# Kernel optimization log

Measured on AMD Instinct MI355X. Metric: run time of the kernel, lower is better.

Reference implementation:

```python
import jax, jax.numpy as jnp
import numpy as np

# Dimensions (match init_kwargs / input_specs)
B, T, D, H, HH, E, L = 256, 512, 256, 256, 128, 32, 2


def setup_inputs() -> dict:
    key = jax.random.key(0)
    ks = jax.random.split(key, 8)
    f32 = jnp.float32
    s_ih = 1.0 / np.sqrt(D)
    s_hh = 1.0 / np.sqrt(H)
    s_hy = 1.0 / np.sqrt(D + H)
    s_hh_hy = 1.0 / np.sqrt(HH)
    s_z = 1.0 / np.sqrt(HH)
    s_d = 1.0 / np.sqrt(E)
    return {
        "input": jax.random.normal(ks[0], (B, T, D), f32),
        # main-cell weights, stacked over layers (layer1 input = hidden = D)
        "Wih": jax.random.normal(ks[1], (L, H, D), f32) * s_ih,
        "Whh": jax.random.normal(ks[2], (L, H, H), f32) * s_hh,
        "b": jnp.zeros((L, H), f32),
        # hyper (meta) RNN cell: input is concat(x_t, h_{t-1})
        "Wih_hy": jax.random.normal(ks[3], (L, HH, D + H), f32) * s_hy,
        "Whh_hy": jax.random.normal(ks[4], (L, HH, HH), f32) * s_hh_hy,
        "b_hy": jnp.zeros((L, HH), f32),
        # embedding projections: hyper_h -> z for (x-scale, h-scale, bias), then z -> d
        "Whz": jax.random.normal(ks[5], (L, 3, E, HH), f32) * s_z,
        "bz": jnp.ones((L, 3, E), f32),  # init z to 1 so d starts near a plain RNN
        "Wzd": jax.random.normal(ks[6], (L, 3, H, E), f32) * s_d,
    }


def reference(input, Wih, Whh, b, Wih_hy, Whh_hy, b_hy, Whz, bz, Wzd):
    """MetaRNN (HyperNetwork-conditioned RNN): for each layer, a small hyper RNN
    consumes [x_t, h_{t-1}] and emits embeddings z that generate per-unit scales
    d_x, d_h and a dynamic bias d_b for the main tanh RNN cell.
    Returns (all hidden states [B,T,H], last hidden state [B,H])."""
    Bb = input.shape[0]
    dt = input.dtype
    x_seq = input
    for l in range(L):
        # input-to-hidden GEMM for the whole sequence, hoisted out of the scan
        xW = jnp.einsum('btd,hd->bth', x_seq, Wih[l])  # [B,T,H]
        Whh_l, b_l = Whh[l], b[l]
        Wih_hy_l, Whh_hy_l, b_hy_l = Wih_hy[l], Whh_hy[l], b_hy[l]
        Whz_l, bz_l, Wzd_l = Whz[l], bz[l], Wzd[l]

        def step(carry, inp):
            h, hh = carry           # main hidden [B,H], hyper hidden [B,HH]
            x_t, xW_t = inp
            hyp_in = jnp.concatenate([x_t, h], axis=1)          # [B, D+H]
            hh_new = jnp.tanh(hyp_in @ Wih_hy_l.T + hh @ Whh_hy_l.T + b_hy_l)
            z = jnp.einsum('bk,gek->bge', hh_new, Whz_l) + bz_l  # [B,3,E]
            d = jnp.einsum('bge,ghe->bgh', z, Wzd_l)             # [B,3,H]
            h_new = jnp.tanh(d[:, 0] * xW_t + d[:, 1] * (h @ Whh_l.T)
                             + d[:, 2] + b_l)
            return (h_new, hh_new), h_new

        h0 = jnp.zeros((Bb, H), dt)
        hh0 = jnp.zeros((Bb, HH), dt)
        xs = (jnp.swapaxes(x_seq, 0, 1), jnp.swapaxes(xW, 0, 1))  # time-major
        _, ys = jax.lax.scan(step, (h0, hh0), xs)
        x_seq = jnp.swapaxes(ys, 0, 1)  # [B,T,H]
    return (x_seq, x_seq[:, -1, :])
```

## Files before the change

### kernel.cpp

```cpp
#include <hip/hip_runtime.h>


#define DEVI __device__ __forceinline__

typedef __bf16 bf16x8 __attribute__((ext_vector_type(8)));
typedef float f32x4 __attribute__((ext_vector_type(4)));
typedef unsigned short u16;
typedef unsigned int u32;
typedef u32 u32x4 __attribute__((ext_vector_type(4)));
typedef u16 u16x8 __attribute__((ext_vector_type(8)));

constexpr int B_ = 256, T_ = 512, D_ = 256, H_ = 256, HH_ = 128, E_ = 32;
constexpr int BT = B_ * T_;

constexpr int OXW = 0,      PXW = 16 * 8 * 512;
constexpr int OXH = 131072, PXH = 8 * 8 * 512;
constexpr int OHY = 196608, PHY = 8 * 12 * 512;
constexpr int OWHH = 294912, PWHH = 16 * 8 * 512;
constexpr int OWHZ = 425984, PWHZ = 6 * 4 * 512;
constexpr int OWZD = 450560, PWZD = 48 * 512;
constexpr int LSTRIDE = 499712;

constexpr size_t WS_XW = 0;
constexpr size_t WS_XH = (size_t)BT * H_ * 4;
constexpr size_t WS_FR = WS_XH + (size_t)BT * HH_ * 4;

DEVI u16 f2bf(float v) {
  u32 u = __float_as_uint(v);
  u += 0x7fffu + ((u >> 16) & 1u);
  return (u16)(u >> 16);
}
DEVI float bf2f(u16 s) { return __uint_as_float(((u32)s) << 16); }
DEVI void split2(float v, u16 &hi, u16 &lo) {
  hi = f2bf(v);
  lo = f2bf(v - bf2f(hi));
}
DEVI bf16x8 ldfrag(const u16 *p) {
  u32x4 v = *reinterpret_cast<const u32x4 *>(p);
  return __builtin_bit_cast(bf16x8, v);
}
DEVI void pin(bf16x8 &x) {
  u32x4 t = __builtin_bit_cast(u32x4, x);
  asm volatile("" : "+v"(t));
  x = __builtin_bit_cast(bf16x8, t);
}
DEVI f32x4 mfma3(bf16x8 ah, bf16x8 al, bf16x8 bh, bf16x8 bl, f32x4 c) {
  c = __builtin_amdgcn_mfma_f32_16x16x32_bf16(ah, bh, c, 0, 0, 0);
  c = __builtin_amdgcn_mfma_f32_16x16x32_bf16(ah, bl, c, 0, 0, 0);
  c = __builtin_amdgcn_mfma_f32_16x16x32_bf16(al, bh, c, 0, 0, 0);
  return c;
}
DEVI float tanh_fast(float x) {
  float e = __expf(2.0f * x);
  return 1.0f - 2.0f / (e + 1.0f);
}
DEVI void block_sync() {
  asm volatile("s_waitcnt lgkmcnt(0)\n\ts_barrier" ::: "memory");
}

__global__ void metarnn_prep(const float *__restrict__ Wih,
                             const float *__restrict__ Whh,
                             const float *__restrict__ Wih_hy,
                             const float *__restrict__ Whh_hy,
                             const float *__restrict__ Whz,
                             const float *__restrict__ Wzd,
                             u16 *__restrict__ fr) {
  int gid = blockIdx.x * 256 + threadIdx.x;
  int lane = gid & 63;
  int e = gid >> 6;
  if (e >= 2 * 488) return;
  int l = e / 488, r = e - l * 488;
  u16 *base = fr + (size_t)l * LSTRIDE;
  int rowL = lane & 15, kg = (lane >> 4) << 3;

  const float *src = nullptr;
  int ld = 0, nt = 0, kt = 0, KT = 1, special = 0;
  u16 *dh = nullptr, *dl = nullptr;
  if (r < 128) {
    nt = r >> 3; kt = r & 7; KT = 8;
    src = Wih + (size_t)l * H_ * D_; ld = D_;
    dh = base + OXW; dl = dh + PXW;
  } else if (r < 192) {
    r -= 128; nt = r >> 3; kt = r & 7; KT = 8;
    src = Wih_hy + (size_t)l * HH_ * (D_ + H_); ld = D_ + H_;
    dh = base + OXH; dl = dh + PXH;
  } else if (r < 288) {
    r -= 192; nt = r / 12; kt = r - nt * 12; KT = 12; special = 1;
    dh = base + OHY; dl = dh + PHY;
  } else if (r < 416) {
    r -= 288; nt = r >> 3; kt = r & 7; KT = 8;
    src = Whh + (size_t)l * H_ * H_; ld = H_;
    dh = base + OWHH; dl = dh + PWHH;
  } else if (r < 440) {
    r -= 416; nt = r >> 2; kt = r & 3; KT = 4;
    src = Whz + (size_t)l * 3 * E_ * HH_; ld = HH_;
    dh = base + OWHZ; dl = dh + PWHZ;
  } else {
    r -= 440; int g = r >> 4; nt = r & 15; kt = 0; KT = 1;
    src = Wzd + (size_t)(l * 3 + g) * H_ * E_; ld = E_;
    dh = base + OWZD + g * 16 * 512; dl = base + OWZD + PWZD + g * 16 * 512;
  }
  int row = nt * 16 + rowL;
  long dof = ((long)(nt * KT + kt) * 64 + lane) * 8;
  for (int j = 0; j < 8; ++j) {
    int k = kt * 32 + kg + j;
    float v;
    if (special) {
      v = (k < 256) ? Wih_hy[((size_t)l * HH_ + row) * (D_ + H_) + 256 + k]
                    : Whh_hy[((size_t)l * HH_ + row) * HH_ + (k - 256)];
    } else {
      v = src[(size_t)row * ld + k];
    }
    u16 hi, lo;
    split2(v, hi, lo);
    dh[dof + j] = hi;
    dl[dof + j] = lo;
  }
}

__global__ __launch_bounds__(256, 1) void metarnn_gemm(
    const float *__restrict__ x, const u16 *__restrict__ fr,
    float *__restrict__ xW, float *__restrict__ xH) {
  int w = threadIdx.x >> 6, lane = threadIdx.x & 63;
  int m0 = blockIdx.x * 32;
  int rowL = lane & 15, kg = (lane >> 4) << 3;
  f32x4 acc[2][6] = {};
  const u16 *fxw_h = fr + OXW, *fxw_l = fxw_h + PXW;
  const u16 *fxh_h = fr + OXH, *fxh_l = fxh_h + PXH;

  for (int kt = 0; kt < 8; ++kt) {
    bf16x8 ah[2], al[2];
    for (int s = 0; s < 2; ++s) {
      const float *xp = x + (size_t)(m0 + s * 16 + rowL) * 256 + kt * 32 + kg;
      u16x8 vh, vl;
#pragma unroll
      for (int j = 0; j < 8; ++j) {
        u16 hi, lo;
        split2(xp[j], hi, lo);
        vh[j] = hi; vl[j] = lo;
      }
      ah[s] = __builtin_bit_cast(bf16x8, vh);
      al[s] = __builtin_bit_cast(bf16x8, vl);
    }
#pragma unroll
    for (int q = 0; q < 6; ++q) {
      int nt = w * 6 + q;
      long o = (nt < 16) ? ((long)(nt * 8 + kt) * 64 + lane) * 8
                         : ((long)((nt - 16) * 8 + kt) * 64 + lane) * 8;
      const u16 *bh = (nt < 16) ? fxw_h + o : fxh_h + o;
      const u16 *bl = (nt < 16) ? fxw_l + o : fxh_l + o;
      bf16x8 B0 = ldfrag(bh), B1 = ldfrag(bl);
      acc[0][q] = mfma3(ah[0], al[0], B0, B1, acc[0][q]);
      acc[1][q] = mfma3(ah[1], al[1], B0, B1, acc[1][q]);
    }
  }
  for (int s = 0; s < 2; ++s)
    for (int q = 0; q < 6; ++q) {
      int nt = w * 6 + q;
#pragma unroll
      for (int r = 0; r < 4; ++r) {
        int row = m0 + s * 16 + (lane >> 4) * 4 + r;
        if (nt < 16)
          xW[(size_t)row * H_ + nt * 16 + rowL] = acc[s][q][r];
        else
          xH[(size_t)row * HH_ + (nt - 16) * 16 + rowL] = acc[s][q][r];
      }
    }
}

__global__ __launch_bounds__(512, 2) void metarnn_scan(
    const float *__restrict__ xW, const float *__restrict__ xH,
    const u16 *__restrict__ fr, const float *__restrict__ bmain,
    const float *__restrict__ bhy, const float *__restrict__ bz,
    float *__restrict__ y, float *__restrict__ hlast, int layer, int isLast) {
  __shared__ __align__(16) u16 hc_h[8 * 512];
  __shared__ __align__(16) u16 hc_l[8 * 512];
  __shared__ __align__(16) u16 hhb_h[2][4 * 512];
  __shared__ __align__(16) u16 hhb_l[2][4 * 512];
  __shared__ __align__(16) u16 zf_h[3 * 512];
  __shared__ __align__(16) u16 zf_l[3 * 512];
  __shared__ __align__(16) u16 hy_lds[8 * 12 * 512];

  int tid = threadIdx.x, w = tid >> 6, lane = tid & 63;
  int bs = blockIdx.x * 16;
  int rowL = lane & 15, colG = lane >> 4;

  const u16 *FHY = fr + OHY, *FHYl = FHY + PHY;
  const u16 *FWH = fr + OWHH, *FWHl = FWH + PWHH;
  const u16 *FWZ = fr + OWHZ, *FWZl = FWZ + PWHZ;
  const u16 *FZD = fr + OWZD, *FZDl = FZD + PWZD;

  for (int i = tid; i < 8 * 512; i += 512) { hc_h[i] = 0; hc_l[i] = 0; }
  for (int i = tid; i < 4 * 512; i += 512) {
    hhb_h[0][i] = 0; hhb_l[0][i] = 0; hhb_h[1][i] = 0; hhb_l[1][i] = 0;
  }
  for (int i = tid; i < 3 * 512; i += 512) { zf_h[i] = 0; zf_l[i] = 0; }
  for (int i = tid; i < 8 * 12 * 512 / 8; i += 512) {
    *reinterpret_cast<u32x4 *>(&hy_lds[(size_t)i * 8]) =
        *reinterpret_cast<const u32x4 *>(FHY + (size_t)i * 8);
  }

  bf16x8 RWH[2][8], RWL[2][8];
#pragma unroll
  for (int p = 0; p < 2; ++p)
#pragma unroll
    for (int kt = 0; kt < 8; ++kt) {
      long o = ((long)((2 * w + p) * 8 + kt) * 64 + lane) * 8;
      RWH[p][kt] = ldfrag(FWH + o);  pin(RWH[p][kt]);
      RWL[p][kt] = ldfrag(FWHl + o); pin(RWL[p][kt]);
    }
  bf16x8 zresH[4], zresL[4];
  {
    int wz = (w < 6) ? w : 0;
#pragma unroll
    for (int kk = 0; kk < 4; ++kk) {
      long o = ((long)(wz * 4 + kk) * 64 + lane) * 8;
      zresH[kk] = ldfrag(FWZ + o);  pin(zresH[kk]);
      zresL[kk] = ldfrag(FWZl + o); pin(zresL[kk]);
    }
  }

  int c2 = 16 * w + rowL;
  float bhv = bhy[layer * HH_ + c2];
  float bzv = (w < 6) ? bz[layer * 3 * E_ + c2] : 0.0f;
  float bbv[2];
  bbv[0] = bmain[layer * H_ + 32 * w + rowL];
  bbv[1] = bmain[layer * H_ + 32 * w + 16 + rowL];

  bf16x8 bYL[4];
#define LOAD_Y(PTR, S, KT)                                                    \
  bYL[S] = ldfrag((PTR) + ((long)(w * 12 + (KT)) * 64 + lane) * 8);
#pragma unroll
  for (int s = 0; s < 4; ++s) { LOAD_Y(FHYl, s, s) }

  float xhv[4], xwv[2][4];
#pragma unroll
  for (int r = 0; r < 4; ++r) {
    size_t row = (size_t)(bs + 4 * colG + r) * T_;
    xhv[r] = xH[row * HH_ + c2];
    xwv[0][r] = xW[row * H_ + 32 * w + rowL];
    xwv[1][r] = xW[row * H_ + 32 * w + 16 + rowL];
  }

  __syncthreads();

  for (int t = 0; t < T_; ++t) {
    const int pr = t & 1;
    const u16 *fhyl = FHYl, *fzd = FZD, *fzdl = FZDl;
    asm volatile("" : "+s"(fhyl), "+s"(fzd), "+s"(fzdl));

    f32x4 aAe = {}, aAo = {}, aW0 = {}, aW1 = {};
    __builtin_amdgcn_s_setprio(1);
#pragma unroll
    for (int j = 0; j < 12; ++j) {
      const int s4 = j & 3;
      bf16x8 ah, al;
      if (j < 8) {
        ah = ldfrag(&hc_h[j * 512 + lane * 8]);
        al = ldfrag(&hc_l[j * 512 + lane * 8]);
      } else {
        ah = ldfrag(&hhb_h[pr ^ 1][(j - 8) * 512 + lane * 8]);
        al = ldfrag(&hhb_l[pr ^ 1][(j - 8) * 512 + lane * 8]);
      }
      bf16x8 yh = ldfrag(&hy_lds[(w * 12 + j) * 512 + lane * 8]);
      if (j & 1) aAo = mfma3(ah, al, yh, bYL[s4], aAo);
      else       aAe = mfma3(ah, al, yh, bYL[s4], aAe);
      if (j < 8) {
        aW0 = mfma3(ah, al, RWH[0][j], RWL[0][j], aW0);
        aW1 = mfma3(ah, al, RWH[1][j], RWL[1][j], aW1);
        LOAD_Y(fhyl, s4, j + 4)
      } else {
        LOAD_Y(fhyl, s4, j - 8)
      }
    }
    __builtin_amdgcn_s_setprio(0);
    f32x4 aA;
#pragma unroll
    for (int r = 0; r < 4; ++r) aA[r] = aAe[r] + aAo[r];

    bf16x8 D0h[2], D0l[2];
#pragma unroll
    for (int p = 0; p < 2; ++p) {
      long o = ((long)(2 * w + p) * 64 + lane) * 8;
      D0h[p] = ldfrag(fzd + o);
      D0l[p] = ldfrag(fzdl + o);
    }

    {
      int kfr = w >> 1;
      int hb2 = 2 * (w & 1) + (rowL >> 3);
      int j7 = rowL & 7;
#pragma unroll
      for (int r = 0; r < 4; ++r) {
        float v = tanh_fast(aA[r] + xhv[r] + bhv);
        u16 hi, lo;
        split2(v, hi, lo);
        int di = kfr * 512 + ((4 * colG + r) + 16 * hb2) * 8 + j7;
        hhb_h[pr][di] = hi;
        hhb_l[pr][di] = lo;
      }
    }
#pragma unroll
    for (int r = 0; r < 4; ++r) {
      xhv[r] = xH[((size_t)(bs + 4 * colG + r) * T_ + t + 1) * HH_ + c2];
    }
    block_sync();

    bf16x8 D1h[2], D1l[2], D2h[2], D2l[2];
#pragma unroll
    for (int p = 0; p < 2; ++p) {
      long o1 = ((long)(16 + 2 * w + p) * 64 + lane) * 8;
      long o2 = ((long)(32 + 2 * w + p) * 64 + lane) * 8;
      D1h[p] = ldfrag(fzd + o1);
      D1l[p] = ldfrag(fzdl + o1);
      D2h[p] = ldfrag(fzd + o2);
      D2l[p] = ldfrag(fzdl + o2);
    }

    if (w < 6) {
      f32x4 aZ = {};
#pragma unroll
      for (int kk = 0; kk < 4; ++kk) {
        bf16x8 ah = ldfrag(&hhb_h[pr][kk * 512 + lane * 8]);
        bf16x8 al = ldfrag(&hhb_l[pr][kk * 512 + lane * 8]);
        aZ = mfma3(ah, al, zresH[kk], zresL[kk], aZ);
      }
      int g = c2 >> 5;
      int hb3 = 2 * (w & 1) + (rowL >> 3);
      int j7 = rowL & 7;
#pragma unroll
      for (int r = 0; r < 4; ++r) {
        float v = aZ[r] + bzv;
        u16 hi, lo;
        split2(v, hi, lo);
        int di = g * 512 + ((4 * colG + r) + 16 * hb3) * 8 + j7;
        zf_h[di] = hi;
        zf_l[di] = lo;
      }
    }
    block_sync();

    float arg[2][4];
#pragma unroll
    for (int p = 0; p < 2; ++p)
#pragma unroll
      for (int r = 0; r < 4; ++r) arg[p][r] = bbv[p];
    {
      bf16x8 zh = ldfrag(&zf_h[0 * 512 + lane * 8]);
      bf16x8 zl = ldfrag(&zf_l[0 * 512 + lane * 8]);
#pragma unroll
      for (int p = 0; p < 2; ++p) {
        f32x4 zero = {};
        f32x4 dg = mfma3(zh, zl, D0h[p], D0l[p], zero);
#pragma unroll
        for (int r = 0; r < 4; ++r) arg[p][r] += dg[r] * xwv[p][r];
      }
    }
#pragma unroll
    for (int r = 0; r < 4; ++r) {
      size_t row = (size_t)(bs + 4 * colG + r) * T_ + t + 1;
      xwv[0][r] = xW[row * H_ + 32 * w + rowL];
      xwv[1][r] = xW[row * H_ + 32 * w + 16 + rowL];
    }
    {
      bf16x8 zh = ldfrag(&zf_h[1 * 512 + lane * 8]);
      bf16x8 zl = ldfrag(&zf_l[1 * 512 + lane * 8]);
#pragma unroll
      for (int p = 0; p < 2; ++p) {
        f32x4 zero = {};
        f32x4 dg = mfma3(zh, zl, D1h[p], D1l[p], zero);
#pragma unroll
        for (int r = 0; r < 4; ++r)
          arg[p][r] += dg[r] * ((p == 0) ? aW0[r] : aW1[r]);
      }
    }
    {
      bf16x8 zh = ldfrag(&zf_h[2 * 512 + lane * 8]);
      bf16x8 zl = ldfrag(&zf_l[2 * 512 + lane * 8]);
#pragma unroll
      for (int p = 0; p < 2; ++p) {
        f32x4 zero = {};
        f32x4 dg = mfma3(zh, zl, D2h[p], D2l[p], zero);
#pragma unroll
        for (int r = 0; r < 4; ++r) arg[p][r] += dg[r];
      }
    }

#pragma unroll
    for (int p = 0; p < 2; ++p) {
      int c = 32 * w + 16 * p + rowL;
      int hb6 = 2 * p + (rowL >> 3);
      int j7 = rowL & 7;
#pragma unroll
      for (int r = 0; r < 4; ++r) {
        int m = 4 * colG + r;
        float h = tanh_fast(arg[p][r]);
        size_t gi = (size_t)(bs + m) * T_ + t;
        y[gi * H_ + c] = h;
        if (isLast && t == T_ - 1) hlast[(size_t)(bs + m) * H_ + c] = h;
        u16 hi, lo;
        split2(h, hi, lo);
        int di = (c >> 5) * 512 + (m + 16 * hb6) * 8 + j7;
        hc_h[di] = hi;
        hc_l[di] = lo;
      }
    }
    block_sync();
  }
#undef LOAD_Y
}

extern "C" void kernel_launch(void *const *d_in, const int *in_sizes, int n_in,
                              void *d_out, int out_size, void *d_ws,
                              size_t ws_size, hipStream_t stream) {
  (void)in_sizes; (void)n_in; (void)out_size; (void)ws_size;
  const float *input  = (const float *)d_in[0];
  const float *Wih    = (const float *)d_in[1];
  const float *Whh    = (const float *)d_in[2];
  const float *b      = (const float *)d_in[3];
  const float *Wih_hy = (const float *)d_in[4];
  const float *Whh_hy = (const float *)d_in[5];
  const float *b_hy   = (const float *)d_in[6];
  const float *Whz    = (const float *)d_in[7];
  const float *bz     = (const float *)d_in[8];
  const float *Wzd    = (const float *)d_in[9];

  float *out = (float *)d_out;
  float *xW = (float *)((char *)d_ws + WS_XW);
  float *xH = (float *)((char *)d_ws + WS_XH);
  u16 *fr = (u16 *)((char *)d_ws + WS_FR);
  float *hlast = out + (size_t)BT * H_;

  metarnn_prep<<<dim3(244), dim3(256), 0, stream>>>(Wih, Whh, Wih_hy, Whh_hy,
                                                    Whz, Wzd, fr);
  for (int l = 0; l < 2; ++l) {
    const float *xsrc = (l == 0) ? input : out;
    const u16 *frl = fr + (size_t)l * LSTRIDE;
    metarnn_gemm<<<dim3(BT / 32), dim3(256), 0, stream>>>(xsrc, frl, xW, xH);
    metarnn_scan<<<dim3(16), dim3(512), 0, stream>>>(
        xW, xH, frl, b, b_hy, bz, out, hlast, l, (l == 1) ? 1 : 0);
  }
}
```

Baseline: 9.273 ms.

## Keep hyper weights in registers, move Whz hi to LDS, split weights inline in gemm

The scan kernel now holds all 12 low-part hyper-RNN weight fragments in registers instead of streaming them from global memory each step. The Whz high part moves into LDS and its low part is reloaded per step rather than pinned, and the Wzd fragment loads are spread across phases to reduce register pressure. The input GEMM now reads fp32 weights directly and splits them into bf16 hi/lo pairs inline, which removes the prep work and workspace for those matrices. This shifts register and LDS budgets inside the latency-bound recurrent loop and adds conversion work to the GEMM.

```diff
diff --git a/kernel.cpp b/kernel.cpp
--- a/kernel.cpp
+++ b/kernel.cpp
@@ -13,13 +13,11 @@
 constexpr int B_ = 256, T_ = 512, D_ = 256, H_ = 256, HH_ = 128, E_ = 32;
 constexpr int BT = B_ * T_;
 
-constexpr int OXW = 0,      PXW = 16 * 8 * 512;
-constexpr int OXH = 131072, PXH = 8 * 8 * 512;
-constexpr int OHY = 196608, PHY = 8 * 12 * 512;
-constexpr int OWHH = 294912, PWHH = 16 * 8 * 512;
-constexpr int OWHZ = 425984, PWHZ = 6 * 4 * 512;
-constexpr int OWZD = 450560, PWZD = 48 * 512;
-constexpr int LSTRIDE = 499712;
+constexpr int OHY = 0,       PHY = 8 * 12 * 512;
+constexpr int OWHH = 98304,  PWHH = 16 * 8 * 512;
+constexpr int OWHZ = 229376, PWHZ = 6 * 4 * 512;
+constexpr int OWZD = 253952, PWZD = 48 * 512;
+constexpr int LSTRIDE = 303104;
 
 constexpr size_t WS_XW = 0;
 constexpr size_t WS_XH = (size_t)BT * H_ * 4;
@@ -58,8 +56,7 @@
   asm volatile("s_waitcnt lgkmcnt(0)\n\ts_barrier" ::: "memory");
 }
 
-__global__ void metarnn_prep(const float *__restrict__ Wih,
-                             const float *__restrict__ Whh,
+__global__ void metarnn_prep(const float *__restrict__ Whh,
                              const float *__restrict__ Wih_hy,
                              const float *__restrict__ Whh_hy,
                              const float *__restrict__ Whz,
@@ -68,65 +65,76 @@
   int gid = blockIdx.x * 256 + threadIdx.x;
   int lane = gid & 63;
   int e = gid >> 6;
-  if (e >= 2 * 488) return;
-  int l = e / 488, r = e - l * 488;
+  if (e >= 2 * 296) return;
+  int l = e / 296, r = e - l * 296;
   u16 *base = fr + (size_t)l * LSTRIDE;
   int rowL = lane & 15, kg = (lane >> 4) << 3;
 
-  const float *src = nullptr;
-  int ld = 0, nt = 0, kt = 0, KT = 1, special = 0;
-  u16 *dh = nullptr, *dl = nullptr;
-  if (r < 128) {
-    nt = r >> 3; kt = r & 7; KT = 8;
-    src = Wih + (size_t)l * H_ * D_; ld = D_;
-    dh = base + OXW; dl = dh + PXW;
-  } else if (r < 192) {
-    r -= 128; nt = r >> 3; kt = r & 7; KT = 8;
-    src = Wih_hy + (size_t)l * HH_ * (D_ + H_); ld = D_ + H_;
-    dh = base + OXH; dl = dh + PXH;
-  } else if (r < 288) {
-    r -= 192; nt = r / 12; kt = r - nt * 12; KT = 12; special = 1;
-    dh = base + OHY; dl = dh + PHY;
-  } else if (r < 416) {
-    r -= 288; nt = r >> 3; kt = r & 7; KT = 8;
-    src = Whh + (size_t)l * H_ * H_; ld = H_;
-    dh = base + OWHH; dl = dh + PWHH;
-  } else if (r < 440) {
-    r -= 416; nt = r >> 2; kt = r & 3; KT = 4;
-    src = Whz + (size_t)l * 3 * E_ * HH_; ld = HH_;
-    dh = base + OWHZ; dl = dh + PWHZ;
+  if (r < 96) {
+    int nt = r / 12, kt = r - nt * 12;
+    u16 *dh = base + OHY, *dl = dh + PHY;
+    int row = nt * 16 + rowL;
+    long dof = ((long)(nt * 12 + kt) * 64 + lane) * 8;
+    for (int j = 0; j < 8; ++j) {
+      int k = kt * 32 + kg + j;
+      float v = (k < 256)
+                    ? Wih_hy[((size_t)l * HH_ + row) * (D_ + H_) + 256 + k]
+                    : Whh_hy[((size_t)l * HH_ + row) * HH_ + (k - 256)];
+      u16 hi, lo;
+      split2(v, hi, lo);
+      dh[dof + j] = hi;
+      dl[dof + j] = lo;
+    }
+  } else if (r < 224) {
+    int m = r - 96;
+    int nt = m >> 3, kt = m & 7;
+    u16 *dh = base + OWHH, *dl = dh + PWHH;
+    int row = nt * 16 + rowL;
+    long dof = ((long)(nt * 8 + kt) * 64 + lane) * 8;
+    const float *src = Whh + (size_t)l * H_ * H_;
+    for (int j = 0; j < 8; ++j) {
+      u16 hi, lo;
+      split2(src[(size_t)row * H_ + kt * 32 + kg + j], hi, lo);
+      dh[dof + j] = hi;
+      dl[dof + j] = lo;
+    }
+  } else if (r < 248) {
+    int m = r - 224;
+    int nt = m >> 2, kt = m & 3;
+    u16 *dh = base + OWHZ, *dl = dh + PWHZ;
+    int row = nt * 16 + rowL;
+    long dof = ((long)(nt * 4 + kt) * 64 + lane) * 8;
+    const float *src = Whz + (size_t)l * 3 * E_ * HH_;
+    for (int j = 0; j < 8; ++j) {
+      u16 hi, lo;
+      split2(src[(size_t)row * HH_ + kt * 32 + kg + j], hi, lo);
+      dh[dof + j] = hi;
+      dl[dof + j] = lo;
+    }
   } else {
-    r -= 440; int g = r >> 4; nt = r & 15; kt = 0; KT = 1;
-    src = Wzd + (size_t)(l * 3 + g) * H_ * E_; ld = E_;
-    dh = base + OWZD + g * 16 * 512; dl = base + OWZD + PWZD + g * 16 * 512;
-  }
-  int row = nt * 16 + rowL;
-  long dof = ((long)(nt * KT + kt) * 64 + lane) * 8;
-  for (int j = 0; j < 8; ++j) {
-    int k = kt * 32 + kg + j;
-    float v;
-    if (special) {
-      v = (k < 256) ? Wih_hy[((size_t)l * HH_ + row) * (D_ + H_) + 256 + k]
-                    : Whh_hy[((size_t)l * HH_ + row) * HH_ + (k - 256)];
-    } else {
-      v = src[(size_t)row * ld + k];
-    }
-    u16 hi, lo;
-    split2(v, hi, lo);
-    dh[dof + j] = hi;
-    dl[dof + j] = lo;
+    int m = r - 248;
+    int g = m >> 4, nt = m & 15;
+    u16 *dh = base + OWZD + g * 16 * 512, *dl = dh + PWZD;
+    int row = nt * 16 + rowL;
+    long dof = ((long)nt * 64 + lane) * 8;
+    const float *src = Wzd + (size_t)(l * 3 + g) * H_ * E_;
+    for (int j = 0; j < 8; ++j) {
+      u16 hi, lo;
+      split2(src[(size_t)row * E_ + kg + j], hi, lo);
+      dh[dof + j] = hi;
+      dl[dof + j] = lo;
+    }
   }
 }
 
 __global__ __launch_bounds__(256, 1) void metarnn_gemm(
-    const float *__restrict__ x, const u16 *__restrict__ fr,
-    float *__restrict__ xW, float *__restrict__ xH) {
+    const float *__restrict__ x, const float *__restrict__ Wih_l,
+    const float *__restrict__ Why_l, float *__restrict__ xW,
+    float *__restrict__ xH) {
   int w = threadIdx.x >> 6, lane = threadIdx.x & 63;
   int m0 = blockIdx.x * 32;
   int rowL = lane & 15, kg = (lane >> 4) << 3;
   f32x4 acc[2][6] = {};
-  const u16 *fxw_h = fr + OXW, *fxw_l = fxw_h + PXW;
-  const u16 *fxh_h = fr + OXH, *fxh_l = fxh_h + PXH;
 
   for (int kt = 0; kt < 8; ++kt) {
     bf16x8 ah[2], al[2];
@@ -145,11 +153,18 @@
 #pragma unroll
     for (int q = 0; q < 6; ++q) {
       int nt = w * 6 + q;
-      long o = (nt < 16) ? ((long)(nt * 8 + kt) * 64 + lane) * 8
-                         : ((long)((nt - 16) * 8 + kt) * 64 + lane) * 8;
-      const u16 *bh = (nt < 16) ? fxw_h + o : fxh_h + o;
-      const u16 *bl = (nt < 16) ? fxw_l + o : fxh_l + o;
-      bf16x8 B0 = ldfrag(bh), B1 = ldfrag(bl);
+      const float *wp = (nt < 16)
+          ? Wih_l + (size_t)(nt * 16 + rowL) * 256 + kt * 32 + kg
+          : Why_l + (size_t)((nt - 16) * 16 + rowL) * 512 + kt * 32 + kg;
+      u16x8 vbh, vbl;
+#pragma unroll
+      for (int j = 0; j < 8; ++j) {
+        u16 hi, lo;
+        split2(wp[j], hi, lo);
+        vbh[j] = hi; vbl[j] = lo;
+      }
+      bf16x8 B0 = __builtin_bit_cast(bf16x8, vbh);
+      bf16x8 B1 = __builtin_bit_cast(bf16x8, vbl);
       acc[0][q] = mfma3(ah[0], al[0], B0, B1, acc[0][q]);
       acc[1][q] = mfma3(ah[1], al[1], B0, B1, acc[1][q]);
     }
@@ -180,6 +195,7 @@
   __shared__ __align__(16) u16 zf_h[3 * 512];
   __shared__ __align__(16) u16 zf_l[3 * 512];
   __shared__ __align__(16) u16 hy_lds[8 * 12 * 512];
+  __shared__ __align__(16) u16 whz_lds[6 * 4 * 512];
 
   int tid = threadIdx.x, w = tid >> 6, lane = tid & 63;
   int bs = blockIdx.x * 16;
@@ -199,6 +215,10 @@
     *reinterpret_cast<u32x4 *>(&hy_lds[(size_t)i * 8]) =
         *reinterpret_cast<const u32x4 *>(FHY + (size_t)i * 8);
   }
+  for (int i = tid; i < 6 * 4 * 512 / 8; i += 512) {
+    *reinterpret_cast<u32x4 *>(&whz_lds[(size_t)i * 8]) =
+        *reinterpret_cast<const u32x4 *>(FWZ + (size_t)i * 8);
+  }
 
   bf16x8 RWH[2][8], RWL[2][8];
 #pragma unroll
@@ -209,30 +229,21 @@
       RWH[p][kt] = ldfrag(FWH + o);  pin(RWH[p][kt]);
       RWL[p][kt] = ldfrag(FWHl + o); pin(RWL[p][kt]);
     }
-  bf16x8 zresH[4], zresL[4];
-  {
-    int wz = (w < 6) ? w : 0;
-#pragma unroll
-    for (int kk = 0; kk < 4; ++kk) {
-      long o = ((long)(wz * 4 + kk) * 64 + lane) * 8;
-      zresH[kk] = ldfrag(FWZ + o);  pin(zresH[kk]);
-      zresL[kk] = ldfrag(FWZl + o); pin(zresL[kk]);
-    }
+  bf16x8 RYL[12];
+#pragma unroll
+  for (int j = 0; j < 12; ++j) {
+    RYL[j] = ldfrag(FHYl + ((long)(w * 12 + j) * 64 + lane) * 8);
+    pin(RYL[j]);
   }
 
   int c2 = 16 * w + rowL;
+  int wz = (w < 6) ? w : 0;
   float bhv = bhy[layer * HH_ + c2];
   float bzv = (w < 6) ? bz[layer * 3 * E_ + c2] : 0.0f;
   float bbv[2];
   bbv[0] = bmain[layer * H_ + 32 * w + rowL];
   bbv[1] = bmain[layer * H_ + 32 * w + 16 + rowL];
 
-  bf16x8 bYL[4];
-#define LOAD_Y(PTR, S, KT)                                                    \
-  bYL[S] = ldfrag((PTR) + ((long)(w * 12 + (KT)) * 64 + lane) * 8);
-#pragma unroll
-  for (int s = 0; s < 4; ++s) { LOAD_Y(FHYl, s, s) }
-
   float xhv[4], xwv[2][4];
 #pragma unroll
   for (int r = 0; r < 4; ++r) {
@@ -246,14 +257,11 @@
 
   for (int t = 0; t < T_; ++t) {
     const int pr = t & 1;
-    const u16 *fhyl = FHYl, *fzd = FZD, *fzdl = FZDl;
-    asm volatile("" : "+s"(fhyl), "+s"(fzd), "+s"(fzdl));
-
+    const int tn = (t + 1 < T_) ? t + 1 : t;
     f32x4 aAe = {}, aAo = {}, aW0 = {}, aW1 = {};
     __builtin_amdgcn_s_setprio(1);
 #pragma unroll
     for (int j = 0; j < 12; ++j) {
-      const int s4 = j & 3;
       bf16x8 ah, al;
       if (j < 8) {
         ah = ldfrag(&hc_h[j * 512 + lane * 8]);
@@ -263,14 +271,11 @@
         al = ldfrag(&hhb_l[pr ^ 1][(j - 8) * 512 + lane * 8]);
       }
       bf16x8 yh = ldfrag(&hy_lds[(w * 12 + j) * 512 + lane * 8]);
-      if (j & 1) aAo = mfma3(ah, al, yh, bYL[s4], aAo);
-      else       aAe = mfma3(ah, al, yh, bYL[s4], aAe);
+      if (j & 1) aAo = mfma3(ah, al, yh, RYL[j], aAo);
+      else       aAe = mfma3(ah, al, yh, RYL[j], aAe);
       if (j < 8) {
         aW0 = mfma3(ah, al, RWH[0][j], RWL[0][j], aW0);
         aW1 = mfma3(ah, al, RWH[1][j], RWL[1][j], aW1);
-        LOAD_Y(fhyl, s4, j + 4)
-      } else {
-        LOAD_Y(fhyl, s4, j - 8)
       }
     }
     __builtin_amdgcn_s_setprio(0);
@@ -278,13 +283,10 @@
 #pragma unroll
     for (int r = 0; r < 4; ++r) aA[r] = aAe[r] + aAo[r];
 
-    bf16x8 D0h[2], D0l[2];
-#pragma unroll
-    for (int p = 0; p < 2; ++p) {
-      long o = ((long)(2 * w + p) * 64 + lane) * 8;
-      D0h[p] = ldfrag(fzd + o);
-      D0l[p] = ldfrag(fzdl + o);
-    }
+    bf16x8 zSl[4];
+#pragma unroll
+    for (int kk = 0; kk < 4; ++kk)
+      zSl[kk] = ldfrag(FWZl + ((long)(wz * 4 + kk) * 64 + lane) * 8);
 
     {
       int kfr = w >> 1;
@@ -302,19 +304,16 @@
     }
 #pragma unroll
     for (int r = 0; r < 4; ++r) {
-      xhv[r] = xH[((size_t)(bs + 4 * colG + r) * T_ + t + 1) * HH_ + c2];
+      xhv[r] = xH[((size_t)(bs + 4 * colG + r) * T_ + tn) * HH_ + c2];
     }
     block_sync();
 
-    bf16x8 D1h[2], D1l[2], D2h[2], D2l[2];
+    bf16x8 D0h[2], D0l[2];
 #pragma unroll
     for (int p = 0; p < 2; ++p) {
-      long o1 = ((long)(16 + 2 * w + p) * 64 + lane) * 8;
-      long o2 = ((long)(32 + 2 * w + p) * 64 + lane) * 8;
-      D1h[p] = ldfrag(fzd + o1);
-      D1l[p] = ldfrag(fzdl + o1);
-      D2h[p] = ldfrag(fzd + o2);
-      D2l[p] = ldfrag(fzdl + o2);
+      long o = ((long)(2 * w + p) * 64 + lane) * 8;
+      D0h[p] = ldfrag(FZD + o);
+      D0l[p] = ldfrag(FZDl + o);
     }
 
     if (w < 6) {
@@ -323,7 +322,8 @@
       for (int kk = 0; kk < 4; ++kk) {
         bf16x8 ah = ldfrag(&hhb_h[pr][kk * 512 + lane * 8]);
         bf16x8 al = ldfrag(&hhb_l[pr][kk * 512 + lane * 8]);
-        aZ = mfma3(ah, al, zresH[kk], zresL[kk], aZ);
+        bf16x8 zh = ldfrag(&whz_lds[(w * 4 + kk) * 512 + lane * 8]);
+        aZ = mfma3(ah, al, zh, zSl[kk], aZ);
       }
       int g = c2 >> 5;
       int hb3 = 2 * (w & 1) + (rowL >> 3);
@@ -340,6 +340,14 @@
     }
     block_sync();
 
+    bf16x8 D1h[2], D1l[2];
+#pragma unroll
+    for (int p = 0; p < 2; ++p) {
+      long o = ((long)(16 + 2 * w + p) * 64 + lane) * 8;
+      D1h[p] = ldfrag(FZD + o);
+      D1l[p] = ldfrag(FZDl + o);
+    }
+
     float arg[2][4];
 #pragma unroll
     for (int p = 0; p < 2; ++p)
@@ -357,8 +365,14 @@
       }
     }
 #pragma unroll
+    for (int p = 0; p < 2; ++p) {
+      long o = ((long)(32 + 2 * w + p) * 64 + lane) * 8;
+      D0h[p] = ldfrag(FZD + o);
+      D0l[p] = ldfrag(FZDl + o);
+    }
+#pragma unroll
     for (int r = 0; r < 4; ++r) {
-      size_t row = (size_t)(bs + 4 * colG + r) * T_ + t + 1;
+      size_t row = (size_t)(bs + 4 * colG + r) * T_ + tn;
       xwv[0][r] = xW[row * H_ + 32 * w + rowL];
       xwv[1][r] = xW[row * H_ + 32 * w + 16 + rowL];
     }
@@ -380,7 +394,7 @@
 #pragma unroll
       for (int p = 0; p < 2; ++p) {
         f32x4 zero = {};
-        f32x4 dg = mfma3(zh, zl, D2h[p], D2l[p], zero);
+        f32x4 dg = mfma3(zh, zl, D0h[p], D0l[p], zero);
 #pragma unroll
         for (int r = 0; r < 4; ++r) arg[p][r] += dg[r];
       }
@@ -407,7 +421,6 @@
     }
     block_sync();
   }
-#undef LOAD_Y
 }
 
 extern "C" void kernel_launch(void *const *d_in, const int *in_sizes, int n_in,
@@ -431,12 +444,14 @@
   u16 *fr = (u16 *)((char *)d_ws + WS_FR);
   float *hlast = out + (size_t)BT * H_;
 
-  metarnn_prep<<<dim3(244), dim3(256), 0, stream>>>(Wih, Whh, Wih_hy, Whh_hy,
-                                                    Whz, Wzd, fr);
+  metarnn_prep<<<dim3(148), dim3(256), 0, stream>>>(Whh, Wih_hy, Whh_hy, Whz,
+                                                    Wzd, fr);
   for (int l = 0; l < 2; ++l) {
     const float *xsrc = (l == 0) ? input : out;
     const u16 *frl = fr + (size_t)l * LSTRIDE;
-    metarnn_gemm<<<dim3(BT / 32), dim3(256), 0, stream>>>(xsrc, frl, xW, xH);
+    metarnn_gemm<<<dim3(BT / 32), dim3(256), 0, stream>>>(
+        xsrc, Wih + (size_t)l * H_ * D_, Wih_hy + (size_t)l * HH_ * (D_ + H_),
+        xW, xH);
     metarnn_scan<<<dim3(16), dim3(512), 0, stream>>>(
         xW, xH, frl, b, b_hy, bz, out, hlast, l, (l == 1) ? 1 : 0);
   }
```

Result: slower. 9.779 ms (+5.5%).
